# Performance work log

Measured on AMD Instinct MI355X. Metric: run time of the kernel, lower is better.

Reference implementation:

```python
import jax, jax.numpy as jnp
import numpy as np
from jax import lax

B, SEQ, CIN = 8, 4096, 7
DM, NL, PL = 512, 4, 16
NP = SEQ // PL            # 256 patches
NS, DC, EXP = 16, 4, 2
DI = EXP * DM             # 1024 inner dim
DTR = (DM + 15) // 16     # 32 dt_rank (mamba_ssm default ceil(d_model/16))
CD, PRED = 64, 96
EPS = 1e-5


def setup_inputs() -> dict:
    key = jax.random.key(0)
    ks = jax.random.split(key, 16)
    r = lambda k, s, sc=0.02: jax.random.normal(k, s, jnp.float32) * sc
    A_row = jnp.arange(1, NS + 1, dtype=jnp.float32)
    return {
        "x": jax.random.normal(ks[0], (B, SEQ, CIN), jnp.float32),
        "in_g": jnp.ones((CIN,), jnp.float32), "in_b": jnp.zeros((CIN,), jnp.float32),
        "pe_W": r(ks[1], (DM, CIN, PL), 0.1), "pe_b": jnp.zeros((DM,), jnp.float32),
        "ln_g": jnp.ones((NL, DM), jnp.float32), "ln_b": jnp.zeros((NL, DM), jnp.float32),
        "W_in": r(ks[2], (NL, 2 * DI, DM)),
        "conv_W": r(ks[3], (NL, DI, 1, DC), 0.2), "conv_b": jnp.zeros((NL, DI), jnp.float32),
        "W_x": r(ks[4], (NL, DTR + 2 * NS, DI)),
        "W_dt": r(ks[5], (NL, DI, DTR), 0.1),
        "b_dt": jnp.full((NL, DI), -4.6, jnp.float32),  # softplus^-1(~0.01)
        "A_log": jnp.log(jnp.tile(A_row, (NL, DI, 1))),
        "Dskip": jnp.ones((NL, DI), jnp.float32),
        "W_out": r(ks[6], (NL, DM, DI)),
        "fn_g": jnp.ones((DM,), jnp.float32), "fn_b": jnp.zeros((DM,), jnp.float32),
        "hW1": r(ks[7], (2 * CD, DM * NP)), "hb1": jnp.zeros((2 * CD,), jnp.float32),
        "hW2": r(ks[8], (PRED, 2 * CD)), "hb2": jnp.zeros((PRED,), jnp.float32),
    }


def layernorm(x, g, b):
    m = jnp.mean(x, axis=-1, keepdims=True)
    v = jnp.mean((x - m) ** 2, axis=-1, keepdims=True)
    return (x - m) * lax.rsqrt(v + EPS) * g + b


def silu(x):
    return x * jax.nn.sigmoid(x)


def selective_scan(dA, dBx, C):
    # dA, dBx: (B, L, DI, N);  C: (B, L, N)  ->  y: (B, L, DI)
    def step(h, t):
        dA_t, dbx_t, c_t = t
        h = dA_t * h + dbx_t                      # (B, DI, N)
        y = jnp.einsum('bdn,bn->bd', h, c_t)
        return h, y
    h0 = jnp.zeros((dA.shape[0], DI, NS), dA.dtype)
    _, ys = lax.scan(step, h0, (dA.transpose(1, 0, 2, 3), dBx.transpose(1, 0, 2, 3), C.transpose(1, 0, 2)))
    return ys.transpose(1, 0, 2)


def mamba_block(u, W_in, cW, cb, W_x, W_dt, b_dt, A_log, Dv, W_out):
    xz = jnp.einsum('bld,ed->ble', u, W_in)       # (B, L, 2*DI)
    xi, z = jnp.split(xz, 2, axis=-1)
    # causal depthwise conv over time
    xc = lax.conv_general_dilated(xi.transpose(0, 2, 1), cW, (1,), [(DC - 1, 0)],
                                  feature_group_count=DI,
                                  dimension_numbers=('NCH', 'OIH', 'NCH'))
    xc = silu(xc + cb[None, :, None]).transpose(0, 2, 1)  # (B, L, DI)
    dbl = jnp.einsum('bld,ed->ble', xc, W_x)      # (B, L, DTR + 2*NS)
    dt, Bm, Cm = dbl[..., :DTR], dbl[..., DTR:DTR + NS], dbl[..., DTR + NS:]
    delta = jax.nn.softplus(jnp.einsum('blr,dr->bld', dt, W_dt) + b_dt)  # (B, L, DI)
    A = -jnp.exp(A_log)                           # (DI, NS)
    dA = jnp.exp(delta[..., None] * A)            # (B, L, DI, NS)
    dBx = delta[..., None] * Bm[:, :, None, :] * xc[..., None]
    y = selective_scan(dA, dBx, Cm)
    y = (y + xc * Dv) * silu(z)
    return jnp.einsum('bld,od->blo', y, W_out)


def reference(x, in_g, in_b, pe_W, pe_b, ln_g, ln_b, W_in, conv_W, conv_b,
              W_x, W_dt, b_dt, A_log, Dskip, W_out, fn_g, fn_b, hW1, hb1, hW2, hb2):
    h = layernorm(x, in_g, in_b)
    # patch embed: stride==kernel Conv1d == per-patch matmul
    p = h.reshape(B, NP, PL, CIN)
    h = jnp.einsum('bnpc,dcp->bnd', p, pe_W) + pe_b   # (B, NP, DM)
    for i in range(NL):
        res = h
        h = layernorm(h, ln_g[i], ln_b[i])
        h = mamba_block(h, W_in[i], conv_W[i], conv_b[i], W_x[i], W_dt[i],
                        b_dt[i], A_log[i], Dskip[i], W_out[i])
        h = h + res                                   # dropout is identity at eval
    h = layernorm(h, fn_g, fn_b)
    h = h.reshape(B, -1)                              # (B, DM*NP)
    h = jax.nn.gelu(h @ hW1.T + hb1, approximate=False)
    return h @ hW2.T + hb2                            # (B, PRED)
```

## Files before the change

kernel.cpp:

```cpp
#include <hip/hip_runtime.h>
#include <hip/hip_bf16.h>
#include <math.h>

#define B_    8
#define SEQ_  4096
#define CIN_  7
#define DM_   512
#define NL_   4
#define PL_   16
#define NP_   256
#define NS_   16
#define DC_   4
#define DI_   1024
#define DTR_  32
#define CD_   64
#define PRED_ 96
#define TOK_  (B_*NP_)
#define EPS_  1e-5f
#define CL_   16
#define NCH_  (NP_/CL_)

typedef unsigned short u16;
typedef __attribute__((ext_vector_type(8))) short short8;
typedef __attribute__((ext_vector_type(4))) float floatx4;

__device__ __forceinline__ float silu_f(float x){ return x / (1.f + __expf(-x)); }
__device__ __forceinline__ float softplus_f(float x){ return x > 20.f ? x : log1pf(__expf(x)); }
__device__ __forceinline__ u16 f2bf(float f){
  union { __hip_bfloat16 h; u16 u; } cv; cv.h = __float2bfloat16(f); return cv.u;
}
#define GLDS16(g, l) __builtin_amdgcn_global_load_lds( \
    (const __attribute__((address_space(1))) void*)(g), \
    (__attribute__((address_space(3))) void*)(l), 16, 0, 0)

__global__ void ln7_kernel(const float* __restrict__ x, const float* __restrict__ g,
                           const float* __restrict__ b, u16* __restrict__ xpb){
  int i = blockIdx.x*256 + threadIdx.x;
  if (i >= B_*SEQ_) return;
  float v[CIN_]; float m = 0.f;
  #pragma unroll
  for (int c=0;c<CIN_;c++){ v[c]=x[i*CIN_+c]; m+=v[c]; }
  m *= (1.f/CIN_);
  float var = 0.f;
  #pragma unroll
  for (int c=0;c<CIN_;c++){ float d=v[c]-m; var+=d*d; }
  var *= (1.f/CIN_);
  float r = rsqrtf(var + EPS_);
  int bn = i >> 4, p = i & 15;
  u16* row = xpb + (size_t)bn*128;
  #pragma unroll
  for (int c=0;c<CIN_;c++) row[c*16+p] = f2bf((v[c]-m)*r*g[c]+b[c]);
  row[112+p] = 0;
}

__global__ __launch_bounds__(256) void ln512_kernel(const float* __restrict__ in,
    const float* __restrict__ g, const float* __restrict__ b,
    float* __restrict__ out, u16* __restrict__ outb){
  int tid = threadIdx.x;
  int wv = tid>>6, lane = tid&63;
  int t = blockIdx.x*4 + wv;
  const float4* row = (const float4*)(in + (size_t)t*DM_);
  float4 v0 = row[lane], v1 = row[64+lane];
  float s = v0.x+v0.y+v0.z+v0.w + v1.x+v1.y+v1.z+v1.w;
  #pragma unroll
  for (int o=1;o<64;o<<=1) s += __shfl_xor(s,o);
  float m = s*(1.f/DM_);
  float d0x=v0.x-m,d0y=v0.y-m,d0z=v0.z-m,d0w=v0.w-m;
  float d1x=v1.x-m,d1y=v1.y-m,d1z=v1.z-m,d1w=v1.w-m;
  float q = d0x*d0x+d0y*d0y+d0z*d0z+d0w*d0w + d1x*d1x+d1y*d1y+d1z*d1z+d1w*d1w;
  #pragma unroll
  for (int o=1;o<64;o<<=1) q += __shfl_xor(q,o);
  float r = rsqrtf(q*(1.f/DM_) + EPS_);
  float4 g0 = ((const float4*)g)[lane], g1 = ((const float4*)g)[64+lane];
  float4 b0 = ((const float4*)b)[lane], b1 = ((const float4*)b)[64+lane];
  float4 o0 = { d0x*r*g0.x+b0.x, d0y*r*g0.y+b0.y, d0z*r*g0.z+b0.z, d0w*r*g0.w+b0.w };
  float4 o1 = { d1x*r*g1.x+b1.x, d1y*r*g1.y+b1.y, d1z*r*g1.z+b1.z, d1w*r*g1.w+b1.w };
  ((float4*)(out + (size_t)t*DM_))[lane]    = o0;
  ((float4*)(out + (size_t)t*DM_))[64+lane] = o1;
  ushort4 p0 = { f2bf(o0.x), f2bf(o0.y), f2bf(o0.z), f2bf(o0.w) };
  ushort4 p1 = { f2bf(o1.x), f2bf(o1.y), f2bf(o1.z), f2bf(o1.w) };
  ((ushort4*)(outb + (size_t)t*DM_))[lane]    = p0;
  ((ushort4*)(outb + (size_t)t*DM_))[64+lane] = p1;
}

template<int BM, int BN, bool ACC, bool BIAS>
__global__ __launch_bounds__(256) void gemm_bf16(const u16* __restrict__ A,
    const u16* __restrict__ Bw, float* __restrict__ C, const float* __restrict__ bias,
    int K, int lda, int ldb, int ldc){
  constexpr int MI = BM/32, NI = BN/32;
  __shared__ __align__(16) u16 As[BM*64];
  __shared__ __align__(16) u16 Bs[BN*64];
  int tid = threadIdx.x;
  int wave = __builtin_amdgcn_readfirstlane(tid>>6);
  int lane = tid&63;
  int wm = wave>>1, wn = wave&1;
  int quad = lane>>4, l16 = lane&15;
  int bm = blockIdx.y*BM, bn = blockIdx.x*BN;
  int r8 = lane>>3, sseg = lane&7;
  int gseg = sseg ^ r8;
  floatx4 acc[MI][NI] = {};
  for (int k0 = 0; k0 < K; k0 += 64){
    #pragma unroll
    for (int r = 0; r < BM/32; r++){
      int rowb = (r*4 + wave)*8;
      const u16* gp = A + (size_t)(bm + rowb + r8)*lda + k0 + gseg*8;
      GLDS16(gp, &As[rowb*64]);
    }
    #pragma unroll
    for (int r = 0; r < BN/32; r++){
      int rowb = (r*4 + wave)*8;
      const u16* gp = Bw + (size_t)(bn + rowb + r8)*ldb + k0 + gseg*8;
      GLDS16(gp, &Bs[rowb*64]);
    }
    __syncthreads();
    #pragma unroll
    for (int kh = 0; kh < 2; kh++){
      short8 af[MI], bfr[NI];
      #pragma unroll
      for (int i = 0; i < MI; i++){
        int row = wm*(BM/2)+i*16+l16;
        af[i] = *(short8*)&As[row*64 + (((kh*4+quad)^(row&7))*8)];
      }
      #pragma unroll
      for (int j = 0; j < NI; j++){
        int row = wn*(BN/2)+j*16+l16;
        bfr[j] = *(short8*)&Bs[row*64 + (((kh*4+quad)^(row&7))*8)];
      }
      #pragma unroll
      for (int i = 0; i < MI; i++)
        #pragma unroll
        for (int j = 0; j < NI; j++)
          acc[i][j] = __builtin_amdgcn_mfma_f32_16x16x32_bf16(af[i], bfr[j], acc[i][j], 0, 0, 0);
    }
    __syncthreads();
  }
  #pragma unroll
  for (int i = 0; i < MI; i++){
    #pragma unroll
    for (int j = 0; j < NI; j++){
      #pragma unroll
      for (int r = 0; r < 4; r++){
        int m  = bm + wm*(BM/2) + i*16 + quad*4 + r;
        int nn = bn + wn*(BN/2) + j*16 + l16;
        float v = acc[i][j][r];
        if (ACC) C[(size_t)m*ldc+nn] += v;
        else     C[(size_t)m*ldc+nn]  = BIAS ? v + bias[nn] : v;
      }
    }
  }
}

__global__ void conv_silu_kernel(const float* __restrict__ xz, const float* __restrict__ cW,
                                 const float* __restrict__ cb, float* __restrict__ xc,
                                 u16* __restrict__ xcb){
  int idx = blockIdx.x*256 + threadIdx.x;
  if (idx >= TOK_*DI_/4) return;
  int c4 = idx & (DI_/4 - 1); int t = idx >> 8;
  int l = t & (NP_-1);
  int c = c4*4;
  float4 acc = *(const float4*)&cb[c];
  float wa[4], wb[4], wc[4], wd[4];
  *(float4*)wa = *(const float4*)&cW[(c+0)*DC_];
  *(float4*)wb = *(const float4*)&cW[(c+1)*DC_];
  *(float4*)wc = *(const float4*)&cW[(c+2)*DC_];
  *(float4*)wd = *(const float4*)&cW[(c+3)*DC_];
  const float* base = xz + (size_t)t*(2*DI_) + c;
  #pragma unroll
  for (int k = 0; k < DC_; k++){
    if (l - 3 + k >= 0){
      float4 xv = *(const float4*)(base + (k-3)*(2*DI_));
      acc.x += xv.x*wa[k];
      acc.y += xv.y*wb[k];
      acc.z += xv.z*wc[k];
      acc.w += xv.w*wd[k];
    }
  }
  acc.x = silu_f(acc.x); acc.y = silu_f(acc.y);
  acc.z = silu_f(acc.z); acc.w = silu_f(acc.w);
  *(float4*)&xc[(size_t)t*DI_ + c] = acc;
  ushort4 pb = { f2bf(acc.x), f2bf(acc.y), f2bf(acc.z), f2bf(acc.w) };
  *(ushort4*)&xcb[(size_t)t*DI_ + c] = pb;
}

__global__ __launch_bounds__(256) void delta_kernel(const float* __restrict__ dbl,
    const float* __restrict__ wdtT, const float* __restrict__ bdt, float* __restrict__ delta){
  __shared__ float sdt[16][DTR_];
  int tid = threadIdx.x;
  int t0 = blockIdx.y*16;
  int d = blockIdx.x*256 + tid;
  for (int i = tid; i < 16*DTR_; i += 256){
    int t = i >> 5, r = i & 31;
    sdt[t][r] = dbl[(size_t)(t0 + t)*64 + r];
  }
  float wv[DTR_];
  #pragma unroll
  for (int r = 0; r < DTR_; r++) wv[r] = wdtT[(size_t)r*DI_ + d];
  float bb = bdt[d];
  __syncthreads();
  #pragma unroll 4
  for (int t = 0; t < 16; t++){
    float acc = bb;
    #pragma unroll
    for (int r = 0; r < DTR_; r++) acc += sdt[t][r]*wv[r];
    delta[(size_t)(t0 + t)*DI_ + d] = softplus_f(acc);
  }
}

__global__ __launch_bounds__(256) void scan_part_kernel(const float* __restrict__ delta,
    const float* __restrict__ xc, const float* __restrict__ dbl,
    const float* __restrict__ Alog, float* __restrict__ hend, float* __restrict__ aprod){
  __shared__ float sBC[CL_][32];
  int tid = threadIdx.x;
  int d = blockIdx.x*256 + tid;
  int bych = blockIdx.y;
  int b = bych >> 4, ch = bych & (NCH_-1);
  int base = b*NP_ + ch*CL_;
  for (int i = tid; i < CL_*32; i += 256){
    int t = i >> 5, c = i & 31;
    sBC[t][c] = dbl[(size_t)(base+t)*64 + 32 + c];
  }
  float A[NS_], h[NS_], pr[NS_];
  #pragma unroll
  for (int k = 0; k < NS_; k++){
    A[k] = -__expf(Alog[(size_t)d*NS_ + k]);
    h[k] = 0.f; pr[k] = 1.f;
  }
  __syncthreads();
  #pragma unroll
  for (int t = 0; t < CL_; t++){
    int row = base + t;
    float de = delta[(size_t)row*DI_ + d];
    float xv = xc[(size_t)row*DI_ + d];
    float cde = de*xv;
    #pragma unroll
    for (int k = 0; k < NS_; k++){
      float a = __expf(de*A[k]);
      h[k] = a*h[k] + cde*sBC[t][k];
      pr[k] *= a;
    }
  }
  size_t o = ((size_t)bych*DI_ + d)*NS_;
  #pragma unroll
  for (int k = 0; k < NS_; k++){ hend[o+k] = h[k]; aprod[o+k] = pr[k]; }
}

__global__ __launch_bounds__(256) void scan_fix_kernel(const float* __restrict__ aprod,
    float* __restrict__ hend){
  int id = blockIdx.x*256 + threadIdx.x;
  int nd = id & (DI_*NS_ - 1);
  int b  = id >> 14;
  float h = 0.f;
  #pragma unroll
  for (int ch = 0; ch < NCH_; ch++){
    size_t idx = (size_t)(b*NCH_ + ch)*(DI_*NS_) + nd;
    float ap = aprod[idx];
    float he = hend[idx];
    hend[idx] = h;
    h = ap*h + he;
  }
}

__global__ __launch_bounds__(256) void scan_final_kernel(const float* __restrict__ delta,
    const float* __restrict__ xc, const float* __restrict__ dbl,
    const float* __restrict__ xz, const float* __restrict__ Dv,
    const float* __restrict__ Alog, const float* __restrict__ hin,
    u16* __restrict__ yb){
  __shared__ float sBC[CL_][32];
  int tid = threadIdx.x;
  int d = blockIdx.x*256 + tid;
  int bych = blockIdx.y;
  int b = bych >> 4, ch = bych & (NCH_-1);
  int base = b*NP_ + ch*CL_;
  for (int i = tid; i < CL_*32; i += 256){
    int t = i >> 5, c = i & 31;
    sBC[t][c] = dbl[(size_t)(base+t)*64 + 32 + c];
  }
  float A[NS_], h[NS_];
  size_t o = ((size_t)bych*DI_ + d)*NS_;
  #pragma unroll
  for (int k = 0; k < NS_; k++){
    A[k] = -__expf(Alog[(size_t)d*NS_ + k]);
    h[k] = hin[o + k];
  }
  float Dvd = Dv[d];
  __syncthreads();
  #pragma unroll
  for (int t = 0; t < CL_; t++){
    int row = base + t;
    float de = delta[(size_t)row*DI_ + d];
    float xv = xc[(size_t)row*DI_ + d];
    float zz = xz[(size_t)row*(2*DI_) + DI_ + d];
    float cde = de*xv;
    float p = 0.f;
    #pragma unroll
    for (int k = 0; k < NS_; k++){
      float a = __expf(de*A[k]);
      h[k] = a*h[k] + cde*sBC[t][k];
      p += h[k]*sBC[t][16+k];
    }
    yb[(size_t)row*DI_ + d] = f2bf((p + xv*Dvd) * silu_f(zz));
  }
}

__global__ __launch_bounds__(256) void head1_kernel(const float* __restrict__ u,
    const float* __restrict__ hW1, float* __restrict__ partial){
  const int KTOT = DM_*NP_;
  int nb = blockIdx.x;
  int kc = blockIdx.y;
  int tid = threadIdx.x;
  int lane = tid & 63, wv = tid >> 6;
  int k = kc*1024 + tid*4;
  float4 uv[8];
  #pragma unroll
  for (int m = 0; m < 8; m++) uv[m] = *(const float4*)&u[(size_t)m*KTOT + k];
  float acc[8][8];
  #pragma unroll
  for (int n = 0; n < 8; n++){
    float4 wv4 = *(const float4*)&hW1[(size_t)(nb*8+n)*KTOT + k];
    #pragma unroll
    for (int m = 0; m < 8; m++)
      acc[n][m] = uv[m].x*wv4.x + uv[m].y*wv4.y + uv[m].z*wv4.z + uv[m].w*wv4.w;
  }
  __shared__ float red[4][64];
  #pragma unroll
  for (int n = 0; n < 8; n++){
    #pragma unroll
    for (int m = 0; m < 8; m++){
      float v = acc[n][m];
      v += __shfl_xor(v,1); v += __shfl_xor(v,2); v += __shfl_xor(v,4);
      v += __shfl_xor(v,8); v += __shfl_xor(v,16); v += __shfl_xor(v,32);
      if (lane == 0) red[wv][n*8+m] = v;
    }
  }
  __syncthreads();
  if (tid < 64){
    float s = red[0][tid] + red[1][tid] + red[2][tid] + red[3][tid];
    int n = tid >> 3, m = tid & 7;
    partial[((size_t)kc*128 + nb*8 + n)*8 + m] = s;
  }
}

__global__ void head_combine_kernel(const float* __restrict__ partial,
    const float* __restrict__ hb1, float* __restrict__ t1){
  int idx = blockIdx.x*256 + threadIdx.x;
  if (idx >= 128*8) return;
  int n = idx >> 3, m = idx & 7;
  float s = hb1[n];
  for (int kc = 0; kc < 128; kc++) s += partial[((size_t)kc*128 + n)*8 + m];
  float ge = 0.5f*s*(1.f + erff(s*0.70710678118f));
  t1[m*128 + n] = ge;
}

__global__ void head2_kernel(const float* __restrict__ t1, const float* __restrict__ hW2,
                             const float* __restrict__ hb2, float* __restrict__ out){
  int idx = blockIdx.x*128 + threadIdx.x;
  if (idx >= B_*PRED_) return;
  int m = idx / PRED_, q = idx % PRED_;
  float s = hb2[q];
  #pragma unroll 16
  for (int k = 0; k < 2*CD_; k++) s += t1[m*128 + k]*hW2[q*128 + k];
  out[idx] = s;
}

__global__ __launch_bounds__(256) void prep_kernel(const float* __restrict__ W_dt,
    const float* __restrict__ W_x, const float* __restrict__ W_in,
    const float* __restrict__ W_out, const float* __restrict__ peW,
    float* __restrict__ wdtT, u16* __restrict__ wxB,
    u16* __restrict__ WinB, u16* __restrict__ WoutB, u16* __restrict__ peWb){
  int idx = blockIdx.x*256 + threadIdx.x;
  {
    float4 v = ((const float4*)W_in)[idx];
    ushort4 o = { f2bf(v.x), f2bf(v.y), f2bf(v.z), f2bf(v.w) };
    ((ushort4*)WinB)[idx] = o;
  }
  if (idx < 524288){
    float4 v = ((const float4*)W_out)[idx];
    ushort4 o = { f2bf(v.x), f2bf(v.y), f2bf(v.z), f2bf(v.w) };
    ((ushort4*)WoutB)[idx] = o;
  }
  if (idx < NL_*64*DI_/4){
    float4 v = ((const float4*)W_x)[idx];
    ushort4 o = { f2bf(v.x), f2bf(v.y), f2bf(v.z), f2bf(v.w) };
    ((ushort4*)wxB)[idx] = o;
  }
  if (idx < NL_*DTR_*DI_){
    int l = idx / (DTR_*DI_); int rem = idx % (DTR_*DI_);
    int r = rem / DI_; int d = rem % DI_;
    wdtT[idx] = W_dt[((size_t)l*DI_ + d)*DTR_ + r];
  }
  if (idx < 512*128){
    int d = idx >> 7, kk = idx & 127;
    peWb[idx] = (kk < 112) ? f2bf(peW[d*112 + kk]) : (u16)0;
  }
}

extern "C" void kernel_launch(void* const* d_in, const int* in_sizes, int n_in,
                              void* d_out, int out_size, void* d_ws, size_t ws_size,
                              hipStream_t stream) {
  const float* x      = (const float*)d_in[0];
  const float* in_g   = (const float*)d_in[1];
  const float* in_b   = (const float*)d_in[2];
  const float* pe_W   = (const float*)d_in[3];
  const float* pe_b   = (const float*)d_in[4];
  const float* ln_g   = (const float*)d_in[5];
  const float* ln_b   = (const float*)d_in[6];
  const float* W_in   = (const float*)d_in[7];
  const float* conv_W = (const float*)d_in[8];
  const float* conv_b = (const float*)d_in[9];
  const float* W_x    = (const float*)d_in[10];
  const float* W_dt   = (const float*)d_in[11];
  const float* b_dt   = (const float*)d_in[12];
  const float* A_log  = (const float*)d_in[13];
  const float* Dskip  = (const float*)d_in[14];
  const float* W_out  = (const float*)d_in[15];
  const float* fn_g   = (const float*)d_in[16];
  const float* fn_b   = (const float*)d_in[17];
  const float* hW1    = (const float*)d_in[18];
  const float* hb1    = (const float*)d_in[19];
  const float* hW2    = (const float*)d_in[20];
  const float* hb2    = (const float*)d_in[21];

  float* ws    = (float*)d_ws;
  float* h     = ws;
  float* un    = h     + 1048576;
  float* xz    = un    + 1048576;
  float* xc    = xz    + 4194304;
  float* dblb  = xc    + 2097152;
  float* delta = dblb  + 131072;
  float* y     = delta + 2097152;
  float* wdtT  = y     + 2097152;
  u16*   wxB   = (u16*)(wdtT + 131072);
  float* bf_rgn= wdtT + 131072 + 131072;
  u16*   unb   = (u16*)bf_rgn;
  u16*   yb    = (u16*)(bf_rgn + 524288);
  u16*   WinB  = (u16*)(bf_rgn + 524288 + 1048576);
  u16*   WoutB = (u16*)(bf_rgn + 524288 + 1048576 + 2097152);
  u16*   peWb  = (u16*)(bf_rgn + 524288 + 1048576 + 2097152 + 1048576);
  float* aprod = bf_rgn + 524288 + 1048576 + 2097152 + 1048576 + 32768;
  float* hend  = y;
  u16*   xcb   = (u16*)y;
  u16*   xpb   = (u16*)y;
  float* partial = xz;
  float* t1      = xz + 262144;

  prep_kernel<<<4096, 256, 0, stream>>>(W_dt, W_x, W_in, W_out, pe_W,
                                        wdtT, wxB, WinB, WoutB, peWb);
  ln7_kernel<<<(B_*SEQ_+255)/256, 256, 0, stream>>>(x, in_g, in_b, xpb);
  gemm_bf16<64,128,false,true><<<dim3(DM_/128, TOK_/64), 256, 0, stream>>>(
      xpb, peWb, h, pe_b, 128, 128, 128, DM_);

  for (int l = 0; l < NL_; l++){
    ln512_kernel<<<TOK_/4, 256, 0, stream>>>(h, ln_g + l*DM_, ln_b + l*DM_, un, unb);
    gemm_bf16<64,128,false,false><<<dim3(2*DI_/128, TOK_/64), 256, 0, stream>>>(
        unb, WinB + (size_t)l*2*DI_*DM_, xz, nullptr, DM_, DM_, DM_, 2*DI_);
    conv_silu_kernel<<<(TOK_*DI_/4)/256, 256, 0, stream>>>(
        xz, conv_W + (size_t)l*DI_*DC_, conv_b + (size_t)l*DI_, xc, xcb);
    gemm_bf16<64,64,false,false><<<dim3(1, TOK_/64), 256, 0, stream>>>(
        xcb, wxB + (size_t)l*64*DI_, dblb, nullptr, DI_, DI_, DI_, 64);
    delta_kernel<<<dim3(DI_/256, TOK_/16), 256, 0, stream>>>(
        dblb, wdtT + (size_t)l*DTR_*DI_, b_dt + (size_t)l*DI_, delta);
    scan_part_kernel<<<dim3(DI_/256, B_*NCH_), 256, 0, stream>>>(
        delta, xc, dblb, A_log + (size_t)l*DI_*NS_, hend, aprod);
    scan_fix_kernel<<<(B_*DI_*NS_)/256, 256, 0, stream>>>(aprod, hend);
    scan_final_kernel<<<dim3(DI_/256, B_*NCH_), 256, 0, stream>>>(
        delta, xc, dblb, xz, Dskip + (size_t)l*DI_, A_log + (size_t)l*DI_*NS_, hend, yb);
    gemm_bf16<64,64,true,false><<<dim3(DM_/64, TOK_/64), 256, 0, stream>>>(
        yb, WoutB + (size_t)l*DM_*DI_, h, nullptr, DI_, DI_, DI_, DM_);
  }

  ln512_kernel<<<TOK_/4, 256, 0, stream>>>(h, fn_g, fn_b, un, unb);
  head1_kernel<<<dim3(16, 128), 256, 0, stream>>>(un, hW1, partial);
  head_combine_kernel<<<4, 256, 0, stream>>>(partial, hb1, t1);
  head2_kernel<<<6, 128, 0, stream>>>(t1, hW2, hb2, (float*)d_out);
}
```

Before: 603.4 us.

## Split x_proj GEMM over K, fold reduction into delta kernel, rework head1

The x_proj GEMM (N=64) previously ran on only 32 blocks. It is now split four ways along K into a dedicated MFMA kernel that writes partial sums. The delta kernel sums these partials, writes dbl, and computes delta for all 1024 channels per 16-token block. The head1 matvec is also restructured so each wave handles one output row over a longer K span, with 64 K-chunks instead of 128, removing the shared-memory reduction. This raises parallelism in a latency-bound small GEMM, at the cost of extra partial-buffer traffic and a fused reduction.

```diff
diff --git a/kernel.cpp b/kernel.cpp
--- a/kernel.cpp
+++ b/kernel.cpp
@@ -150,6 +150,62 @@
   }
 }
 
+__global__ __launch_bounds__(256) void dblpart_kernel(const u16* __restrict__ A,
+    const u16* __restrict__ Bw, float* __restrict__ part){
+  __shared__ __align__(16) u16 As[64*64];
+  __shared__ __align__(16) u16 Bs[64*64];
+  int tid = threadIdx.x;
+  int wave = __builtin_amdgcn_readfirstlane(tid>>6);
+  int lane = tid&63;
+  int wm = wave>>1, wn = wave&1;
+  int quad = lane>>4, l16 = lane&15;
+  int bm = blockIdx.x*64;
+  int kc = blockIdx.y;
+  int r8 = lane>>3, sseg = lane&7;
+  int gseg = sseg ^ r8;
+  floatx4 acc[2][2] = {};
+  for (int k0 = kc*256; k0 < kc*256 + 256; k0 += 64){
+    #pragma unroll
+    for (int r = 0; r < 2; r++){
+      int rowb = (r*4 + wave)*8;
+      GLDS16(A  + (size_t)(bm + rowb + r8)*DI_ + k0 + gseg*8, &As[rowb*64]);
+      GLDS16(Bw + (size_t)(     rowb + r8)*DI_ + k0 + gseg*8, &Bs[rowb*64]);
+    }
+    __syncthreads();
+    #pragma unroll
+    for (int kh = 0; kh < 2; kh++){
+      short8 af[2], bfr[2];
+      #pragma unroll
+      for (int i = 0; i < 2; i++){
+        int row = wm*32+i*16+l16;
+        af[i] = *(short8*)&As[row*64 + (((kh*4+quad)^(row&7))*8)];
+      }
+      #pragma unroll
+      for (int j = 0; j < 2; j++){
+        int row = wn*32+j*16+l16;
+        bfr[j] = *(short8*)&Bs[row*64 + (((kh*4+quad)^(row&7))*8)];
+      }
+      #pragma unroll
+      for (int i = 0; i < 2; i++)
+        #pragma unroll
+        for (int j = 0; j < 2; j++)
+          acc[i][j] = __builtin_amdgcn_mfma_f32_16x16x32_bf16(af[i], bfr[j], acc[i][j], 0, 0, 0);
+    }
+    __syncthreads();
+  }
+  float* dst = part + (size_t)kc*TOK_*64;
+  #pragma unroll
+  for (int i = 0; i < 2; i++)
+    #pragma unroll
+    for (int j = 0; j < 2; j++)
+      #pragma unroll
+      for (int r = 0; r < 4; r++){
+        int m  = bm + wm*32 + i*16 + quad*4 + r;
+        int nn = wn*32 + j*16 + l16;
+        dst[(size_t)m*64+nn] = acc[i][j][r];
+      }
+}
+
 __global__ void conv_silu_kernel(const float* __restrict__ xz, const float* __restrict__ cW,
                                  const float* __restrict__ cb, float* __restrict__ xc,
                                  u16* __restrict__ xcb){
@@ -182,27 +238,36 @@
   *(ushort4*)&xcb[(size_t)t*DI_ + c] = pb;
 }
 
-__global__ __launch_bounds__(256) void delta_kernel(const float* __restrict__ dbl,
-    const float* __restrict__ wdtT, const float* __restrict__ bdt, float* __restrict__ delta){
-  __shared__ float sdt[16][DTR_];
-  int tid = threadIdx.x;
-  int t0 = blockIdx.y*16;
-  int d = blockIdx.x*256 + tid;
-  for (int i = tid; i < 16*DTR_; i += 256){
-    int t = i >> 5, r = i & 31;
-    sdt[t][r] = dbl[(size_t)(t0 + t)*64 + r];
-  }
-  float wv[DTR_];
-  #pragma unroll
-  for (int r = 0; r < DTR_; r++) wv[r] = wdtT[(size_t)r*DI_ + d];
-  float bb = bdt[d];
+__global__ __launch_bounds__(256) void delta_kernel(const float* __restrict__ part,
+    const float* __restrict__ wdtT, const float* __restrict__ bdt,
+    float* __restrict__ dbl, float* __restrict__ delta){
+  __shared__ float sdbl[16][64];
+  int tid = threadIdx.x;
+  int t0 = blockIdx.x*16;
+  #pragma unroll
+  for (int i = tid; i < 16*64; i += 256){
+    int t = i >> 6, e = i & 63;
+    size_t o = (size_t)(t0 + t)*64 + e;
+    float s = part[o] + part[(size_t)TOK_*64 + o]
+            + part[(size_t)2*TOK_*64 + o] + part[(size_t)3*TOK_*64 + o];
+    sdbl[t][e] = s;
+    dbl[o] = s;
+  }
   __syncthreads();
-  #pragma unroll 4
-  for (int t = 0; t < 16; t++){
-    float acc = bb;
-    #pragma unroll
-    for (int r = 0; r < DTR_; r++) acc += sdt[t][r]*wv[r];
-    delta[(size_t)(t0 + t)*DI_ + d] = softplus_f(acc);
+  #pragma unroll
+  for (int dc = 0; dc < 4; dc++){
+    int d = dc*256 + tid;
+    float wr[DTR_];
+    #pragma unroll
+    for (int r = 0; r < DTR_; r++) wr[r] = wdtT[(size_t)r*DI_ + d];
+    float bb = bdt[d];
+    #pragma unroll
+    for (int t = 0; t < 16; t++){
+      float acc = bb;
+      #pragma unroll
+      for (int r = 0; r < DTR_; r++) acc += sdbl[t][r]*wr[r];
+      delta[(size_t)(t0 + t)*DI_ + d] = softplus_f(acc);
+    }
   }
 }
 
@@ -309,34 +374,31 @@
   int kc = blockIdx.y;
   int tid = threadIdx.x;
   int lane = tid & 63, wv = tid >> 6;
-  int k = kc*1024 + tid*4;
-  float4 uv[8];
-  #pragma unroll
-  for (int m = 0; m < 8; m++) uv[m] = *(const float4*)&u[(size_t)m*KTOT + k];
-  float acc[8][8];
-  #pragma unroll
-  for (int n = 0; n < 8; n++){
-    float4 wv4 = *(const float4*)&hW1[(size_t)(nb*8+n)*KTOT + k];
-    #pragma unroll
-    for (int m = 0; m < 8; m++)
-      acc[n][m] = uv[m].x*wv4.x + uv[m].y*wv4.y + uv[m].z*wv4.z + uv[m].w*wv4.w;
-  }
-  __shared__ float red[4][64];
-  #pragma unroll
-  for (int n = 0; n < 8; n++){
+  int n = nb*4 + wv;
+  const float* wrow = hW1 + (size_t)n*KTOT;
+  float acc[8] = {};
+  int kb = kc*2048 + lane*4;
+  #pragma unroll
+  for (int it = 0; it < 8; it++){
+    int k = kb + it*256;
+    float4 w4 = *(const float4*)&wrow[k];
     #pragma unroll
     for (int m = 0; m < 8; m++){
-      float v = acc[n][m];
-      v += __shfl_xor(v,1); v += __shfl_xor(v,2); v += __shfl_xor(v,4);
-      v += __shfl_xor(v,8); v += __shfl_xor(v,16); v += __shfl_xor(v,32);
-      if (lane == 0) red[wv][n*8+m] = v;
-    }
-  }
-  __syncthreads();
-  if (tid < 64){
-    float s = red[0][tid] + red[1][tid] + red[2][tid] + red[3][tid];
-    int n = tid >> 3, m = tid & 7;
-    partial[((size_t)kc*128 + nb*8 + n)*8 + m] = s;
+      float4 u4 = *(const float4*)&u[(size_t)m*KTOT + k];
+      acc[m] += u4.x*w4.x + u4.y*w4.y + u4.z*w4.z + u4.w*w4.w;
+    }
+  }
+  #pragma unroll
+  for (int m = 0; m < 8; m++){
+    float v = acc[m];
+    v += __shfl_xor(v,1); v += __shfl_xor(v,2); v += __shfl_xor(v,4);
+    v += __shfl_xor(v,8); v += __shfl_xor(v,16); v += __shfl_xor(v,32);
+    acc[m] = v;
+  }
+  if (lane == 0){
+    float* dst = partial + ((size_t)kc*128 + n)*8;
+    #pragma unroll
+    for (int m = 0; m < 8; m++) dst[m] = acc[m];
   }
 }
 
@@ -346,7 +408,7 @@
   if (idx >= 128*8) return;
   int n = idx >> 3, m = idx & 7;
   float s = hb1[n];
-  for (int kc = 0; kc < 128; kc++) s += partial[((size_t)kc*128 + n)*8 + m];
+  for (int kc = 0; kc < 64; kc++) s += partial[((size_t)kc*128 + n)*8 + m];
   float ge = 0.5f*s*(1.f + erff(s*0.70710678118f));
   t1[m*128 + n] = ge;
 }
@@ -440,6 +502,7 @@
   float* hend  = y;
   u16*   xcb   = (u16*)y;
   u16*   xpb   = (u16*)y;
+  float* dblpart = aprod;
   float* partial = xz;
   float* t1      = xz + 262144;
 
@@ -455,10 +518,10 @@
         unb, WinB + (size_t)l*2*DI_*DM_, xz, nullptr, DM_, DM_, DM_, 2*DI_);
     conv_silu_kernel<<<(TOK_*DI_/4)/256, 256, 0, stream>>>(
         xz, conv_W + (size_t)l*DI_*DC_, conv_b + (size_t)l*DI_, xc, xcb);
-    gemm_bf16<64,64,false,false><<<dim3(1, TOK_/64), 256, 0, stream>>>(
-        xcb, wxB + (size_t)l*64*DI_, dblb, nullptr, DI_, DI_, DI_, 64);
-    delta_kernel<<<dim3(DI_/256, TOK_/16), 256, 0, stream>>>(
-        dblb, wdtT + (size_t)l*DTR_*DI_, b_dt + (size_t)l*DI_, delta);
+    dblpart_kernel<<<dim3(TOK_/64, 4), 256, 0, stream>>>(
+        xcb, wxB + (size_t)l*64*DI_, dblpart);
+    delta_kernel<<<TOK_/16, 256, 0, stream>>>(
+        dblpart, wdtT + (size_t)l*DTR_*DI_, b_dt + (size_t)l*DI_, dblb, delta);
     scan_part_kernel<<<dim3(DI_/256, B_*NCH_), 256, 0, stream>>>(
         delta, xc, dblb, A_log + (size_t)l*DI_*NS_, hend, aprod);
     scan_fix_kernel<<<(B_*DI_*NS_)/256, 256, 0, stream>>>(aprod, hend);
@@ -469,7 +532,7 @@
   }
 
   ln512_kernel<<<TOK_/4, 256, 0, stream>>>(h, fn_g, fn_b, un, unb);
-  head1_kernel<<<dim3(16, 128), 256, 0, stream>>>(un, hW1, partial);
+  head1_kernel<<<dim3(32, 64), 256, 0, stream>>>(un, hW1, partial);
   head_combine_kernel<<<4, 256, 0, stream>>>(partial, hb1, t1);
   head2_kernel<<<6, 128, 0, stream>>>(t1, hW2, hb2, (float*)d_out);
 }
```

Result: slower. 656.5 us (+8.8%).
